# Performance work log

Hardware: AMD Instinct MI355X
Metric: run time of the kernel (lower is better)

The kernel has to match this reference:

```python
import jax, jax.numpy as jnp
import numpy as np

H = 1024   # hidden size
E = 8      # num experts
B, S = 4, 2048


def setup_inputs() -> dict:
    key = jax.random.key(0)
    k1, k2, k3, k4 = jax.random.split(key, 4)
    x = jax.random.normal(k1, (B, S, H), dtype=jnp.float32)
    wg = jax.random.normal(k2, (H, E), dtype=jnp.float32) * 0.02      # gate weight
    W = jax.random.normal(k3, (E, H, H), dtype=jnp.float32) * 0.02    # expert Linear weights (out, in) per expert
    b = jax.random.normal(k4, (E, H), dtype=jnp.float32) * 0.02       # expert Linear biases
    return {"x": x, "wg": wg, "W": W, "b": b}


def reference(x, wg, W, b):
    Bb, Ss, Hh = x.shape
    Ee = wg.shape[1]
    T = Bb * Ss
    C = T // Ee  # capacity (capacity_factor = 1.0, top-1)

    xt = x.reshape(T, Hh)
    logits = xt @ wg                                   # [T, E]
    probs = jax.nn.softmax(logits, axis=-1)            # [T, E]
    idx = jnp.argmax(probs, axis=-1)                   # [T] top-1 expert
    mask = jax.nn.one_hot(idx, Ee, dtype=xt.dtype)     # [T, E]

    # position of each token within its expert's queue (0-based)
    locations = jnp.cumsum(mask, axis=0) - mask        # [T, E]
    # drop tokens over capacity
    mask = mask * (locations < C).astype(xt.dtype)
    gate = jnp.sum(probs * mask, axis=-1)              # [T] gate prob (0 if dropped)
    loc_s = jnp.sum(locations * mask, axis=-1).astype(jnp.int32)  # [T]
    loc_oh = jax.nn.one_hot(loc_s, C, dtype=xt.dtype)  # [T, C]

    dispatch = mask[:, :, None] * loc_oh[:, None, :]   # [T, E, C]
    combine = gate[:, None, None] * dispatch           # [T, E, C]

    # dispatch tokens -> per-expert buffers [E, C, H]
    exp_in = jnp.einsum('tec,th->ech', dispatch, xt)
    # per-expert Linear: y = x @ W_e^T + b_e
    exp_out = jnp.einsum('ech,efh->ecf', exp_in, W) + b[:, None, :]
    # combine back to tokens, scaled by gate prob
    out = jnp.einsum('tec,ecf->tf', combine, exp_out)  # [T, H]
    return out.reshape(Bb, Ss, Hh)
```

## Files before the change

### kernel.cpp

```cpp
#include <hip/hip_runtime.h>

#define H 1024
#define E 8
#define T 8192
#define CAP 1024

typedef __bf16 bf16x8 __attribute__((ext_vector_type(8)));
typedef float  f32x4  __attribute__((ext_vector_type(4)));
typedef unsigned short u16;

__device__ __forceinline__ u16 f2bf(float f) {
    union { float f; unsigned u; } v; v.f = f;
    unsigned r = v.u + 0x7FFFu + ((v.u >> 16) & 1u);
    return (u16)(r >> 16);
}

typedef __attribute__((address_space(1))) const void* gas_t;
typedef __attribute__((address_space(3))) void* las_t;
__device__ __forceinline__ void gld16(const void* g, void* l) {
    __builtin_amdgcn_global_load_lds((gas_t)g, (las_t)l, 16, 0, 0);
}

#define GATE_BLOCKS 512
#define CVT_BLOCKS  1536

__global__ __launch_bounds__(256) void gatecvt_kernel(
    const float* __restrict__ x, const float* __restrict__ wg,
    const float* __restrict__ W,
    int* __restrict__ eid, float* __restrict__ gate,
    u16* __restrict__ xbf, u16* __restrict__ Wbf) {
    const int tid = threadIdx.x;

    if (blockIdx.x >= GATE_BLOCKS) {
        int i = (blockIdx.x - GATE_BLOCKS) * 256 + tid;
        const int n4 = E * H * H / 4;
        const int stride = CVT_BLOCKS * 256;
        for (; i < n4; i += stride) {
            float4 v = ((const float4*)W)[i];
            ushort4 o;
            o.x = f2bf(v.x); o.y = f2bf(v.y); o.z = f2bf(v.z); o.w = f2bf(v.w);
            ((ushort4*)Wbf)[i] = o;
        }
        return;
    }

    const int wv = tid >> 6, lane = tid & 63;
    const int tbase = blockIdx.x * 16 + wv * 4;
    const int h00 = lane * 4;

    float a[4][8];
    #pragma unroll
    for (int j = 0; j < 4; ++j)
        #pragma unroll
        for (int e = 0; e < 8; ++e) a[j][e] = 0.f;

    #pragma unroll
    for (int q = 0; q < 4; ++q) {
        const int h0 = q * 256 + h00;
        float4 xv[4];
        #pragma unroll
        for (int j = 0; j < 4; ++j)
            xv[j] = *(const float4*)(x + (size_t)(tbase + j) * H + h0);
        #pragma unroll
        for (int j = 0; j < 4; ++j) {
            ushort4 o;
            o.x = f2bf(xv[j].x); o.y = f2bf(xv[j].y);
            o.z = f2bf(xv[j].z); o.w = f2bf(xv[j].w);
            *(ushort4*)(xbf + (size_t)(tbase + j) * H + h0) = o;
        }
        float wr[4][8];
        #pragma unroll
        for (int r = 0; r < 4; ++r) {
            const float4* p = (const float4*)(wg + (size_t)(h0 + r) * E);
            float4 lo = p[0], hi = p[1];
            wr[r][0] = lo.x; wr[r][1] = lo.y; wr[r][2] = lo.z; wr[r][3] = lo.w;
            wr[r][4] = hi.x; wr[r][5] = hi.y; wr[r][6] = hi.z; wr[r][7] = hi.w;
        }
        #pragma unroll
        for (int e = 0; e < 8; ++e)
            #pragma unroll
            for (int j = 0; j < 4; ++j)
                a[j][e] += xv[j].x * wr[0][e] + xv[j].y * wr[1][e]
                         + xv[j].z * wr[2][e] + xv[j].w * wr[3][e];
    }

    const bool b0 = lane & 1, b1 = lane & 2, b2 = lane & 4;
    const int elane = ((lane & 1) << 2) | (lane & 2) | ((lane >> 2) & 1);

    #pragma unroll
    for (int j = 0; j < 4; ++j) {
        float* A = a[j];
        #pragma unroll
        for (int k = 0; k < 4; ++k) {
            float t = b0 ? A[k] : A[k + 4];
            t = __shfl_xor(t, 1);
            A[k] = (b0 ? A[k + 4] : A[k]) + t;
        }
        #pragma unroll
        for (int k = 0; k < 2; ++k) {
            float t = b1 ? A[k] : A[k + 2];
            t = __shfl_xor(t, 2);
            A[k] = (b1 ? A[k + 2] : A[k]) + t;
        }
        {
            float t = b2 ? A[0] : A[1];
            t = __shfl_xor(t, 4);
            A[0] = (b2 ? A[1] : A[0]) + t;
        }
        float v = A[0];
        v += __shfl_xor(v, 8); v += __shfl_xor(v, 16); v += __shfl_xor(v, 32);
        float m = v; int mi = elane;
        #pragma unroll
        for (int off = 1; off <= 4; off <<= 1) {
            float om = __shfl_xor(m, off);
            int   oi = __shfl_xor(mi, off);
            if (om > m || (om == m && oi < mi)) { m = om; mi = oi; }
        }
        float s = expf(v - m);
        s += __shfl_xor(s, 1); s += __shfl_xor(s, 2); s += __shfl_xor(s, 4);
        if (lane == 0) {
            eid[tbase + j]  = mi;
            gate[tbase + j] = 1.0f / s;
        }
    }
}

#define SCAN_T 1024
#define STPT 8
__global__ __launch_bounds__(1024) void scan_kernel(
    const int* __restrict__ eid, float* __restrict__ gate,
    int* __restrict__ perm) {
    __shared__ int cnt[SCAN_T][E];
    __shared__ int part[E][32];
    const int tid = threadIdx.x;

    for (int i = tid; i < E * CAP; i += SCAN_T) perm[i] = -1;

    const int t0 = tid * STPT;
    int ei[STPT];
    #pragma unroll
    for (int i = 0; i < STPT; ++i) ei[i] = eid[t0 + i];

    int c[E];
    #pragma unroll
    for (int e = 0; e < E; ++e) c[e] = 0;
    #pragma unroll
    for (int i = 0; i < STPT; ++i)
        #pragma unroll
        for (int e = 0; e < E; ++e) c[e] += (ei[i] == e);
    #pragma unroll
    for (int e = 0; e < E; ++e) cnt[tid][e] = c[e];
    __syncthreads();

    if (tid < 256) {
        const int e = tid >> 5, g = tid & 31;
        int s = 0;
        for (int i = g * 32; i < g * 32 + 32; ++i) s += cnt[i][e];
        part[e][g] = s;
    }
    __syncthreads();
    if (tid < E) {
        int run = 0;
        #pragma unroll
        for (int g = 0; g < 32; ++g) { int v = part[tid][g]; part[tid][g] = run; run += v; }
    }
    __syncthreads();
    if (tid < 256) {
        const int e = tid >> 5, g = tid & 31;
        int run = part[e][g];
        for (int i = g * 32; i < g * 32 + 32; ++i) { int v = cnt[i][e]; cnt[i][e] = run; run += v; }
    }
    __syncthreads();

    #pragma unroll
    for (int e = 0; e < E; ++e) c[e] = cnt[tid][e];
    #pragma unroll
    for (int i = 0; i < STPT; ++i) {
        const int t = t0 + i, e0 = ei[i];
        int pos = 0;
        #pragma unroll
        for (int k = 0; k < E; ++k) if (e0 == k) pos = c[k]++;
        if (pos < CAP) perm[e0 * CAP + pos] = t;
        else gate[t] = 0.f;
    }
}

__global__ __launch_bounds__(512, 4) void moe_gemm_bf(
    const u16* __restrict__ xbf, const u16* __restrict__ Wbf,
    const float* __restrict__ bias, const int* __restrict__ perm,
    const float* __restrict__ gate, float* __restrict__ out) {
    __shared__ __align__(16) u16 As[2][128 * 64];
    __shared__ __align__(16) u16 Bs[2][128 * 64];
    __shared__ int   perm_s[128];
    __shared__ float gate_s[128];

    const int tid = threadIdx.x;
    const int bid = blockIdx.x;

    if (bid < 64) {
        const int t = bid * 128 + (tid >> 2);
        if (gate[t] == 0.f) {
            const int part = tid & 3;
            float4 z = make_float4(0.f, 0.f, 0.f, 0.f);
            float4* o = (float4*)(out + (size_t)t * H + part * 256);
            #pragma unroll
            for (int i = 0; i < 64; ++i) o[i] = z;
        }
        return;
    }

    const int idx = bid - 64;
    const int e  = idx & 7;
    const int mb = (idx >> 3) & 7;
    const int fb = idx >> 6;

    if (tid < 128) {
        const int t = perm[e * CAP + mb * 128 + tid];
        perm_s[tid] = t;
        gate_s[tid] = (t >= 0) ? gate[t] : 0.f;
    }
    __syncthreads();

    const int lane = tid & 63;
    const int wv = tid >> 6;
    const int wm = wv >> 2;
    const int wn = wv & 3;
    const int l16 = lane & 15, quad = lane >> 4;

    const int rl  = lane >> 3;
    const int cch = lane & 7;
    const int gch = cch ^ rl;
    const u16* ga[2];
    const u16* gb[2];
    #pragma unroll
    for (int q = 0; q < 2; ++q) {
        const int r = wv * 16 + q * 8 + rl;
        const int tA = perm_s[r];
        const int tok = tA >= 0 ? tA : 0;
        ga[q] = xbf + (size_t)tok * H + gch * 8;
        gb[q] = Wbf + (size_t)e * H * H + (size_t)(fb * 128 + r) * H + gch * 8;
    }

#define STAGE(BUF)                                                            \
    {                                                                         \
        _Pragma("unroll")                                                     \
        for (int q = 0; q < 2; ++q) {                                         \
            gld16(ga[q], &As[BUF][(wv * 16 + q * 8) * 64 + lane * 8]);        \
            gld16(gb[q], &Bs[BUF][(wv * 16 + q * 8) * 64 + lane * 8]);        \
        }                                                                     \
        _Pragma("unroll")                                                     \
        for (int q = 0; q < 2; ++q) { ga[q] += 64; gb[q] += 64; }             \
    }

    f32x4 acc[4][2] = {};

    STAGE(0)
    asm volatile("s_waitcnt vmcnt(0)" ::: "memory");
    __builtin_amdgcn_sched_barrier(0);
    __builtin_amdgcn_s_barrier();
    __builtin_amdgcn_sched_barrier(0);

    int p = 0;
    #pragma unroll 1
    for (int t = 0; t < 16; ++t) {
        if (t < 15) STAGE(p ^ 1)

        const u16* cA = As[p];
        const u16* cB = Bs[p];
        __builtin_amdgcn_s_setprio(1);
        #pragma unroll
        for (int kh = 0; kh < 2; ++kh) {
            bf16x8 af[4], bfr[2];
            const int cc = (kh * 4 + quad) ^ (l16 & 7);
            #pragma unroll
            for (int i = 0; i < 4; ++i)
                af[i] = *(const bf16x8*)&cA[(wm * 64 + i * 16 + l16) * 64 + cc * 8];
            #pragma unroll
            for (int i = 0; i < 2; ++i)
                bfr[i] = *(const bf16x8*)&cB[(wn * 32 + i * 16 + l16) * 64 + cc * 8];
            #pragma unroll
            for (int mi = 0; mi < 4; ++mi)
                #pragma unroll
                for (int ni = 0; ni < 2; ++ni)
                    acc[mi][ni] = __builtin_amdgcn_mfma_f32_16x16x32_bf16(
                        af[mi], bfr[ni], acc[mi][ni], 0, 0, 0);
        }
        __builtin_amdgcn_s_setprio(0);
        if (t == 15) break;

        __builtin_amdgcn_sched_barrier(0);
        asm volatile("s_waitcnt vmcnt(0)" ::: "memory");
        __builtin_amdgcn_sched_barrier(0);
        __builtin_amdgcn_s_barrier();
        __builtin_amdgcn_sched_barrier(0);
        p ^= 1;
    }
#undef STAGE

    float bv[2];
    #pragma unroll
    for (int ni = 0; ni < 2; ++ni)
        bv[ni] = bias[e * H + fb * 128 + wn * 32 + ni * 16 + l16];

    #pragma unroll
    for (int mi = 0; mi < 4; ++mi) {
        #pragma unroll
        for (int r = 0; r < 4; ++r) {
            const int rowl = wm * 64 + mi * 16 + quad * 4 + r;
            const int t = perm_s[rowl];
            if (t < 0) continue;
            const float g = gate_s[rowl];
            float* orow = out + (size_t)t * H + fb * 128 + wn * 32;
            #pragma unroll
            for (int ni = 0; ni < 2; ++ni)
                orow[ni * 16 + l16] = g * (acc[mi][ni][r] + bv[ni]);
        }
    }
}

extern "C" void kernel_launch(void* const* d_in, const int* in_sizes, int n_in,
                              void* d_out, int out_size, void* d_ws, size_t ws_size,
                              hipStream_t stream) {
    const float* x    = (const float*)d_in[0];
    const float* wg   = (const float*)d_in[1];
    const float* W    = (const float*)d_in[2];
    const float* bias = (const float*)d_in[3];
    float* out = (float*)d_out;

    int*   eid  = (int*)d_ws;
    float* gate = (float*)((char*)d_ws + (size_t)T * 4);
    int*   perm = (int*)((char*)d_ws + (size_t)T * 8);
    u16*   xbf  = (u16*)((char*)d_ws + (size_t)T * 12);
    u16*   Wbf  = xbf + (size_t)T * H;

    gatecvt_kernel<<<GATE_BLOCKS + CVT_BLOCKS, 256, 0, stream>>>(
        x, wg, W, eid, gate, xbf, Wbf);
    scan_kernel<<<1, SCAN_T, 0, stream>>>(eid, gate, perm);
    moe_gemm_bf<<<64 + 512, 512, 0, stream>>>(xbf, Wbf, bias, perm, gate, out);
}
```

Before: 156.0 us.

## Fuse weight fp32-to-bf16 conversion into GEMM B-tile loads

Removes the separate pass that converted all expert weights to bf16 before the GEMM. The GEMM now loads fp32 weight tiles into registers, converts them with packed bf16 conversion instructions, and writes them to shared memory, while the activation tile still uses direct global-to-LDS loads. This removes a full read-write pass over the weights but doubles per-tile weight bytes read by the GEMM, and register staging adds latency and register pressure.

```diff
diff --git a/kernel.cpp b/kernel.cpp
--- a/kernel.cpp
+++ b/kernel.cpp
@@ -15,35 +15,22 @@
     return (u16)(r >> 16);
 }
 
+__device__ __forceinline__ unsigned cvt2bf(float lo, float hi) {
+    unsigned r;
+    asm("v_cvt_pk_bf16_f32 %0, %1, %2" : "=v"(r) : "v"(lo), "v"(hi));
+    return r;
+}
+
 typedef __attribute__((address_space(1))) const void* gas_t;
 typedef __attribute__((address_space(3))) void* las_t;
 __device__ __forceinline__ void gld16(const void* g, void* l) {
     __builtin_amdgcn_global_load_lds((gas_t)g, (las_t)l, 16, 0, 0);
 }
 
-#define GATE_BLOCKS 512
-#define CVT_BLOCKS  1536
-
-__global__ __launch_bounds__(256) void gatecvt_kernel(
+__global__ __launch_bounds__(256) void gate_kernel(
     const float* __restrict__ x, const float* __restrict__ wg,
-    const float* __restrict__ W,
-    int* __restrict__ eid, float* __restrict__ gate,
-    u16* __restrict__ xbf, u16* __restrict__ Wbf) {
+    int* __restrict__ eid, float* __restrict__ gate, u16* __restrict__ xbf) {
     const int tid = threadIdx.x;
-
-    if (blockIdx.x >= GATE_BLOCKS) {
-        int i = (blockIdx.x - GATE_BLOCKS) * 256 + tid;
-        const int n4 = E * H * H / 4;
-        const int stride = CVT_BLOCKS * 256;
-        for (; i < n4; i += stride) {
-            float4 v = ((const float4*)W)[i];
-            ushort4 o;
-            o.x = f2bf(v.x); o.y = f2bf(v.y); o.z = f2bf(v.z); o.w = f2bf(v.w);
-            ((ushort4*)Wbf)[i] = o;
-        }
-        return;
-    }
-
     const int wv = tid >> 6, lane = tid & 63;
     const int tbase = blockIdx.x * 16 + wv * 4;
     const int h00 = lane * 4;
@@ -186,7 +173,7 @@
 }
 
 __global__ __launch_bounds__(512, 4) void moe_gemm_bf(
-    const u16* __restrict__ xbf, const u16* __restrict__ Wbf,
+    const u16* __restrict__ xbf, const float* __restrict__ W,
     const float* __restrict__ bias, const int* __restrict__ perm,
     const float* __restrict__ gate, float* __restrict__ out) {
     __shared__ __align__(16) u16 As[2][128 * 64];
@@ -230,32 +217,50 @@
     const int rl  = lane >> 3;
     const int cch = lane & 7;
     const int gch = cch ^ rl;
-    const u16* ga[2];
-    const u16* gb[2];
+    const u16*   ga[2];
+    const float* gb[2];
     #pragma unroll
     for (int q = 0; q < 2; ++q) {
         const int r = wv * 16 + q * 8 + rl;
         const int tA = perm_s[r];
         const int tok = tA >= 0 ? tA : 0;
         ga[q] = xbf + (size_t)tok * H + gch * 8;
-        gb[q] = Wbf + (size_t)e * H * H + (size_t)(fb * 128 + r) * H + gch * 8;
-    }
-
-#define STAGE(BUF)                                                            \
-    {                                                                         \
-        _Pragma("unroll")                                                     \
-        for (int q = 0; q < 2; ++q) {                                         \
-            gld16(ga[q], &As[BUF][(wv * 16 + q * 8) * 64 + lane * 8]);        \
-            gld16(gb[q], &Bs[BUF][(wv * 16 + q * 8) * 64 + lane * 8]);        \
-        }                                                                     \
-        _Pragma("unroll")                                                     \
-        for (int q = 0; q < 2; ++q) { ga[q] += 64; gb[q] += 64; }             \
+        gb[q] = W + (size_t)e * H * H + (size_t)(fb * 128 + r) * H + gch * 8;
     }
 
     f32x4 acc[4][2] = {};
-
-    STAGE(0)
-    asm volatile("s_waitcnt vmcnt(0)" ::: "memory");
+    float4 nb[2][2];
+
+#define ISSUE(BUF)                                                           \
+    {                                                                        \
+        _Pragma("unroll")                                                    \
+        for (int q = 0; q < 2; ++q) {                                        \
+            const float4* p4 = (const float4*)gb[q];                         \
+            nb[q][0] = p4[0]; nb[q][1] = p4[1];                              \
+        }                                                                    \
+        _Pragma("unroll")                                                    \
+        for (int q = 0; q < 2; ++q)                                          \
+            gld16(ga[q], &As[BUF][(wv * 16 + q * 8) * 64 + lane * 8]);       \
+        _Pragma("unroll")                                                    \
+        for (int q = 0; q < 2; ++q) { ga[q] += 64; gb[q] += 64; }            \
+    }
+
+#define WRITEB(BUF)                                                          \
+    {                                                                        \
+        _Pragma("unroll")                                                    \
+        for (int q = 0; q < 2; ++q) {                                        \
+            uint4 v;                                                         \
+            v.x = cvt2bf(nb[q][0].x, nb[q][0].y);                            \
+            v.y = cvt2bf(nb[q][0].z, nb[q][0].w);                            \
+            v.z = cvt2bf(nb[q][1].x, nb[q][1].y);                            \
+            v.w = cvt2bf(nb[q][1].z, nb[q][1].w);                            \
+            *(uint4*)&Bs[BUF][(wv * 16 + q * 8 + rl) * 64 + cch * 8] = v;    \
+        }                                                                    \
+    }
+
+    ISSUE(0)
+    WRITEB(0)
+    asm volatile("s_waitcnt vmcnt(0) lgkmcnt(0)" ::: "memory");
     __builtin_amdgcn_sched_barrier(0);
     __builtin_amdgcn_s_barrier();
     __builtin_amdgcn_sched_barrier(0);
@@ -263,7 +268,8 @@
     int p = 0;
     #pragma unroll 1
     for (int t = 0; t < 16; ++t) {
-        if (t < 15) STAGE(p ^ 1)
+        if (t < 15) ISSUE(p ^ 1)
+        __builtin_amdgcn_sched_barrier(0);
 
         const u16* cA = As[p];
         const u16* cB = Bs[p];
@@ -289,13 +295,16 @@
         if (t == 15) break;
 
         __builtin_amdgcn_sched_barrier(0);
-        asm volatile("s_waitcnt vmcnt(0)" ::: "memory");
+        WRITEB(p ^ 1)
+        __builtin_amdgcn_sched_barrier(0);
+        asm volatile("s_waitcnt vmcnt(0) lgkmcnt(0)" ::: "memory");
         __builtin_amdgcn_sched_barrier(0);
         __builtin_amdgcn_s_barrier();
         __builtin_amdgcn_sched_barrier(0);
         p ^= 1;
     }
-#undef STAGE
+#undef ISSUE
+#undef WRITEB
 
     float bv[2];
     #pragma unroll
@@ -331,10 +340,8 @@
     float* gate = (float*)((char*)d_ws + (size_t)T * 4);
     int*   perm = (int*)((char*)d_ws + (size_t)T * 8);
     u16*   xbf  = (u16*)((char*)d_ws + (size_t)T * 12);
-    u16*   Wbf  = xbf + (size_t)T * H;
-
-    gatecvt_kernel<<<GATE_BLOCKS + CVT_BLOCKS, 256, 0, stream>>>(
-        x, wg, W, eid, gate, xbf, Wbf);
+
+    gate_kernel<<<T / 16, 256, 0, stream>>>(x, wg, eid, gate, xbf);
     scan_kernel<<<1, SCAN_T, 0, stream>>>(eid, gate, perm);
-    moe_gemm_bf<<<64 + 512, 512, 0, stream>>>(xbf, Wbf, bias, perm, gate, out);
-}
+    moe_gemm_bf<<<64 + 512, 512, 0, stream>>>(xbf, W, bias, perm, gate, out);
+}
```

After: 166.0 us. 1.06x slower.

## Restructure MoE GEMM to 256 threads with triple-buffered BK=32 pipeline

Applied to the files above, without the earlier changes.

Halves the GEMM block to four waves, each now computing a 64x64 sub-tile with 4x4 MFMA accumulators instead of 64x32. The K tile shrinks from 64 to 32 and the LDS ring grows from two buffers to three, so two loads stay in flight and the wait uses vmcnt(4) rather than draining fully every step. The aim is more register reuse per wave and better overlap of global-to-LDS loads with MFMA work. The cost is twice as many loop iterations and barriers, plus more accumulator registers, which may reduce occupancy.

```diff
diff --git a/kernel.cpp b/kernel.cpp
--- a/kernel.cpp
+++ b/kernel.cpp
@@ -185,12 +185,12 @@
     }
 }
 
-__global__ __launch_bounds__(512, 4) void moe_gemm_bf(
+__global__ __launch_bounds__(256, 3) void moe_gemm_bf(
     const u16* __restrict__ xbf, const u16* __restrict__ Wbf,
     const float* __restrict__ bias, const int* __restrict__ perm,
     const float* __restrict__ gate, float* __restrict__ out) {
-    __shared__ __align__(16) u16 As[2][128 * 64];
-    __shared__ __align__(16) u16 Bs[2][128 * 64];
+    __shared__ __align__(16) u16 As[3][128 * 32];
+    __shared__ __align__(16) u16 Bs[3][128 * 32];
     __shared__ int   perm_s[128];
     __shared__ float gate_s[128];
 
@@ -198,13 +198,13 @@
     const int bid = blockIdx.x;
 
     if (bid < 64) {
-        const int t = bid * 128 + (tid >> 2);
+        const int t = bid * 128 + (tid >> 1);
         if (gate[t] == 0.f) {
-            const int part = tid & 3;
+            const int part = tid & 1;
             float4 z = make_float4(0.f, 0.f, 0.f, 0.f);
-            float4* o = (float4*)(out + (size_t)t * H + part * 256);
+            float4* o = (float4*)(out + (size_t)t * H + part * 512);
             #pragma unroll
-            for (int i = 0; i < 64; ++i) o[i] = z;
+            for (int i = 0; i < 128; ++i) o[i] = z;
         }
         return;
     }
@@ -223,84 +223,86 @@
 
     const int lane = tid & 63;
     const int wv = tid >> 6;
-    const int wm = wv >> 2;
-    const int wn = wv & 3;
+    const int wm = wv >> 1;
+    const int wn = wv & 1;
     const int l16 = lane & 15, quad = lane >> 4;
 
-    const int rl  = lane >> 3;
-    const int cch = lane & 7;
-    const int gch = cch ^ rl;
+    const int srow = tid >> 2;
+    const int cch  = tid & 3;
+    const int gch  = cch ^ (srow & 3);
+
     const u16* ga[2];
     const u16* gb[2];
     #pragma unroll
     for (int q = 0; q < 2; ++q) {
-        const int r = wv * 16 + q * 8 + rl;
+        const int r = q * 64 + srow;
         const int tA = perm_s[r];
         const int tok = tA >= 0 ? tA : 0;
         ga[q] = xbf + (size_t)tok * H + gch * 8;
         gb[q] = Wbf + (size_t)e * H * H + (size_t)(fb * 128 + r) * H + gch * 8;
     }
 
-#define STAGE(BUF)                                                            \
-    {                                                                         \
-        _Pragma("unroll")                                                     \
-        for (int q = 0; q < 2; ++q) {                                         \
-            gld16(ga[q], &As[BUF][(wv * 16 + q * 8) * 64 + lane * 8]);        \
-            gld16(gb[q], &Bs[BUF][(wv * 16 + q * 8) * 64 + lane * 8]);        \
-        }                                                                     \
-        _Pragma("unroll")                                                     \
-        for (int q = 0; q < 2; ++q) { ga[q] += 64; gb[q] += 64; }             \
-    }
-
-    f32x4 acc[4][2] = {};
-
-    STAGE(0)
-    asm volatile("s_waitcnt vmcnt(0)" ::: "memory");
+#define ISSUE(BUF)                                                           \
+    {                                                                        \
+        _Pragma("unroll")                                                    \
+        for (int q = 0; q < 2; ++q) {                                        \
+            gld16(ga[q], &As[BUF][q * 2048 + tid * 8]);                      \
+            gld16(gb[q], &Bs[BUF][q * 2048 + tid * 8]);                      \
+        }                                                                    \
+        _Pragma("unroll")                                                    \
+        for (int q = 0; q < 2; ++q) { ga[q] += 32; gb[q] += 32; }            \
+    }
+
+    f32x4 acc[4][4] = {};
+
+    ISSUE(0)
+    ISSUE(1)
+    asm volatile("s_waitcnt vmcnt(4)" ::: "memory");
     __builtin_amdgcn_sched_barrier(0);
     __builtin_amdgcn_s_barrier();
     __builtin_amdgcn_sched_barrier(0);
 
     int p = 0;
     #pragma unroll 1
-    for (int t = 0; t < 16; ++t) {
-        if (t < 15) STAGE(p ^ 1)
+    for (int t = 0; t < 32; ++t) {
+        int nx = p + 2; if (nx >= 3) nx -= 3;
+        if (t < 30) ISSUE(nx)
+        __builtin_amdgcn_sched_barrier(0);
 
         const u16* cA = As[p];
         const u16* cB = Bs[p];
+        const int cc = quad ^ (l16 & 3);
+        bf16x8 af[4], bf[4];
         __builtin_amdgcn_s_setprio(1);
         #pragma unroll
-        for (int kh = 0; kh < 2; ++kh) {
-            bf16x8 af[4], bfr[2];
-            const int cc = (kh * 4 + quad) ^ (l16 & 7);
+        for (int i = 0; i < 4; ++i)
+            af[i] = *(const bf16x8*)&cA[(wm * 64 + i * 16 + l16) * 32 + cc * 8];
+        #pragma unroll
+        for (int i = 0; i < 4; ++i)
+            bf[i] = *(const bf16x8*)&cB[(wn * 64 + i * 16 + l16) * 32 + cc * 8];
+        #pragma unroll
+        for (int mi = 0; mi < 4; ++mi)
             #pragma unroll
-            for (int i = 0; i < 4; ++i)
-                af[i] = *(const bf16x8*)&cA[(wm * 64 + i * 16 + l16) * 64 + cc * 8];
-            #pragma unroll
-            for (int i = 0; i < 2; ++i)
-                bfr[i] = *(const bf16x8*)&cB[(wn * 32 + i * 16 + l16) * 64 + cc * 8];
-            #pragma unroll
-            for (int mi = 0; mi < 4; ++mi)
-                #pragma unroll
-                for (int ni = 0; ni < 2; ++ni)
-                    acc[mi][ni] = __builtin_amdgcn_mfma_f32_16x16x32_bf16(
-                        af[mi], bfr[ni], acc[mi][ni], 0, 0, 0);
-        }
+            for (int ni = 0; ni < 4; ++ni)
+                acc[mi][ni] = __builtin_amdgcn_mfma_f32_16x16x32_bf16(
+                    af[mi], bf[ni], acc[mi][ni], 0, 0, 0);
         __builtin_amdgcn_s_setprio(0);
-        if (t == 15) break;
+        if (t == 31) break;
 
         __builtin_amdgcn_sched_barrier(0);
-        asm volatile("s_waitcnt vmcnt(0)" ::: "memory");
+        if (t < 30) asm volatile("s_waitcnt vmcnt(4)" ::: "memory");
+        else        asm volatile("s_waitcnt vmcnt(0)" ::: "memory");
         __builtin_amdgcn_sched_barrier(0);
         __builtin_amdgcn_s_barrier();
         __builtin_amdgcn_sched_barrier(0);
-        p ^= 1;
-    }
-#undef STAGE
-
-    float bv[2];
-    #pragma unroll
-    for (int ni = 0; ni < 2; ++ni)
-        bv[ni] = bias[e * H + fb * 128 + wn * 32 + ni * 16 + l16];
+        p = (p == 2) ? 0 : p + 1;
+    }
+#undef ISSUE
+
+    float bv[4];
+    #pragma unroll
+    for (int ni = 0; ni < 4; ++ni)
+        bv[ni] = bias[e * H + fb * 128 + wn * 64 + ni * 16 + l16];
 
     #pragma unroll
     for (int mi = 0; mi < 4; ++mi) {
@@ -310,9 +312,9 @@
             const int t = perm_s[rowl];
             if (t < 0) continue;
             const float g = gate_s[rowl];
-            float* orow = out + (size_t)t * H + fb * 128 + wn * 32;
+            float* orow = out + (size_t)t * H + fb * 128 + wn * 64;
             #pragma unroll
-            for (int ni = 0; ni < 2; ++ni)
+            for (int ni = 0; ni < 4; ++ni)
                 orow[ni * 16 + l16] = g * (acc[mi][ni][r] + bv[ni]);
         }
     }
@@ -336,5 +338,5 @@
     gatecvt_kernel<<<GATE_BLOCKS + CVT_BLOCKS, 256, 0, stream>>>(
         x, wg, W, eid, gate, xbf, Wbf);
     scan_kernel<<<1, SCAN_T, 0, stream>>>(eid, gate, perm);
-    moe_gemm_bf<<<64 + 512, 512, 0, stream>>>(xbf, Wbf, bias, perm, gate, out);
-}
+    moe_gemm_bf<<<64 + 512, 256, 0, stream>>>(xbf, Wbf, bias, perm, gate, out);
+}
```

After: 160.7 us. +3.0%, slower.
